# Optimization experiments

Measured on AMD Instinct MI355X. Metric: run time of the kernel, lower is better.

Reference implementation:

```python
import jax, jax.numpy as jnp
import numpy as np

FS = 30.0        # sampling rate (Hz)
HIGH_PASS = 40.0 # BPM
LOW_PASS = 250.0 # BPM


def setup_inputs() -> dict:
    key = jax.random.key(0)
    k1, k2 = jax.random.split(key)
    B, N = 1024, 16384
    outputs = jax.random.normal(k1, (B, N), dtype=jnp.float32)
    # heart rates in BPM, within (high_pass, low_pass) band so slices are non-degenerate
    targets = 45.0 + 150.0 * jax.random.uniform(k2, (B, 1), dtype=jnp.float32)
    return {"outputs": outputs, "targets": targets}


def reference(outputs, targets):
    N = outputs.shape[-1]
    F = N // 2 + 1
    pulse_band = jnp.array([HIGH_PASS / 60.0, LOW_PASS / 60.0], dtype=jnp.float32)
    f = jnp.linspace(0.0, FS / 2.0, F, dtype=jnp.float32)  # [F]
    min_idx = jnp.argmin(jnp.abs(f - pulse_band[0]))
    max_idx = jnp.argmin(jnp.abs(f - pulse_band[1]))

    outputs = outputs.reshape(-1, N)
    if targets.shape[-1] != 1:
        targets = jnp.mean(targets, axis=-1, keepdims=True)
    t_hz = targets.reshape(-1) / 60.0  # [B] target frequency in Hz

    # rfft with norm='forward' divides by N, matching torch.fft.rfft(norm='forward')
    X = jnp.fft.rfft(outputs, axis=-1, norm='forward')  # [B, F] complex
    P1 = X.real ** 2 + X.imag ** 2                       # [B, F] power spectrum

    # per-sample index of the reference (ground-truth) frequency bin
    ref_idx = jnp.argmin(jnp.abs(f[None, :] - t_hz[:, None]), axis=-1)  # [B]

    # vectorized masked reduction replacing the per-sample python loop:
    # sum over [min_idx, ref_idx-1) U [ref_idx+2, max_idx)
    j = jnp.arange(F)
    ri = ref_idx[:, None]
    mask = ((j[None, :] >= min_idx) & (j[None, :] < ri - 1)) | \
           ((j[None, :] >= ri + 2) & (j[None, :] < max_idx))
    other_sum = jnp.sum(jnp.where(mask, P1, 0.0), axis=-1)              # [B]
    denom = (max_idx - min_idx - 3).astype(jnp.float32)
    other_avrg = other_sum / denom

    pulse_freq_amp = jnp.take_along_axis(P1, ref_idx[:, None], axis=-1)[:, 0]  # [B]
    snrs = 10.0 * jnp.log10(pulse_freq_amp / other_avrg)
    return -jnp.mean(snrs)
```

## Files before the change

### kernel.cpp

```cpp
#include <hip/hip_runtime.h>
#include <math.h>

#define THREADS 512
#define MHALF 8192
#define NREAL 16384
#define MIN_IDX 364
#define MAX_IDX 2276

__device__ __forceinline__ int br13(int x) {
    return (int)(__brev((unsigned)x) >> 19);
}

__device__ __forceinline__ int PHI(int p) {
    return p ^ (((p >> 7) & 7) << 1);
}

__device__ __forceinline__ float2 wtw(float f) {
    return make_float2(__builtin_amdgcn_cosf(f), -__builtin_amdgcn_sinf(f));
}

__device__ __forceinline__ float2 cmul(float2 a, float2 b) {
    return make_float2(a.x * b.x - a.y * b.y, a.x * b.y + a.y * b.x);
}

__device__ __forceinline__ void bfly(float2& a, float2& b, float2 tw) {
    float2 t = make_float2(a.x - b.x, a.y - b.y);
    a.x += b.x; a.y += b.y;
    b = cmul(t, tw);
}

__device__ __forceinline__ void fft_block16(float2 v[16], float2 W1)
{
    constexpr float C16x[8] = {1.f,  0.92387953251128674f,  0.70710678118654757f,  0.38268343236508978f,
                               0.f, -0.38268343236508978f, -0.70710678118654757f, -0.92387953251128674f};
    constexpr float C16y[8] = {0.f, -0.38268343236508978f, -0.70710678118654757f, -0.92387953251128674f,
                              -1.f, -0.92387953251128674f, -0.70710678118654757f, -0.38268343236508978f};
    constexpr float C8x[4] = {1.f,  0.70710678118654757f,  0.f, -0.70710678118654757f};
    constexpr float C8y[4] = {0.f, -0.70710678118654757f, -1.f, -0.70710678118654757f};

    float2 W2 = cmul(W1, W1), W4 = cmul(W2, W2), W8 = cmul(W4, W4);

    #pragma unroll
    for (int m = 0; m < 8; ++m) {
        float2 tw = cmul(W1, make_float2(C16x[m], C16y[m]));
        bfly(v[m], v[m + 8], tw);
    }
    #pragma unroll
    for (int g = 0; g < 2; ++g) {
        #pragma unroll
        for (int m = 0; m < 4; ++m) {
            float2 tw = cmul(W2, make_float2(C8x[m], C8y[m]));
            bfly(v[8 * g + m], v[8 * g + m + 4], tw);
        }
    }
    float2 W4i = make_float2(W4.y, -W4.x);
    #pragma unroll
    for (int g = 0; g < 4; ++g) {
        bfly(v[4 * g + 0], v[4 * g + 2], W4);
        bfly(v[4 * g + 1], v[4 * g + 3], W4i);
    }
    #pragma unroll
    for (int g = 0; g < 8; ++g)
        bfly(v[2 * g], v[2 * g + 1], W8);
}

__global__ __launch_bounds__(THREADS, 2)
void negsnr_row_kernel(const float* __restrict__ x,
                       const float* __restrict__ targets,
                       float* __restrict__ snr_out)
{
    __shared__ float2 cf[MHALF];
    const int row  = blockIdx.x;
    const int tid  = threadIdx.x;
    const int lane = tid & 63;
    const int wave = tid >> 6;

    const float2* xr = (const float2*)(x + (size_t)row * NREAL);
    float2 v[16];
    #pragma unroll
    for (int m = 0; m < 16; ++m) v[m] = xr[tid + 512 * m];

    const float step = 15.0f / 8192.0f;
    const float t_hz = targets[row] / 60.0f;
    int ri;
    {
        int kf = (int)floorf(t_hz * (8192.0f / 15.0f));
        float best = 1e30f; ri = 0;
        #pragma unroll
        for (int d = -1; d <= 2; ++d) {
            int k = min(max(kf + d, 0), 8192);
            float dist = fabsf((float)k * step - t_hz);
            if (dist < best) { best = dist; ri = k; }
        }
    }

    fft_block16(v, wtw((float)tid * (1.0f / 8192.0f)));
    #pragma unroll
    for (int m = 0; m < 16; ++m) cf[PHI(tid + 512 * m)] = v[m];
    __syncthreads();

    const int low5 = tid & 31;
    const int base2 = low5 + ((tid >> 5) << 9);
    #pragma unroll
    for (int m = 0; m < 16; ++m) v[m] = cf[PHI(base2 + 32 * m)];
    fft_block16(v, wtw((float)low5 * (1.0f / 512.0f)));
    #pragma unroll
    for (int m = 0; m < 16; ++m) cf[PHI(base2 + 32 * m)] = v[m];
    __syncthreads();

    const int p = tid & 1;
    const int base3 = p + ((tid >> 1) << 5);
    #pragma unroll
    for (int m = 0; m < 16; ++m) v[m] = cf[PHI(base3 + 2 * m)];
    {
        float2 U = p ? make_float2(0.98078528040323044f, -0.19509032201612825f)
                     : make_float2(1.0f, 0.0f);
        fft_block16(v, U);
    }
    #pragma unroll
    for (int m = 0; m < 16; ++m) cf[PHI(base3 + 2 * m)] = v[m];
    __syncthreads();

    float other = 0.0f, pulse = 0.0f;
    bool hasp = false;
    for (int k = MIN_IDX + tid; k < MAX_IDX; k += THREADS) {
        int a = br13(k);
        int b = br13(MHALF - k);
        float4 ya = *(const float4*)&cf[PHI(a)];
        float4 yb = *(const float4*)&cf[PHI(b - 1)];
        float Zr  = ya.x + ya.z, Zi  = ya.y + ya.w;
        float Zmr = yb.x - yb.z, Zmi = yb.y - yb.w;
        float xer  = 0.5f * (Zr + Zmr), xei = 0.5f * (Zi - Zmi);
        float xor_ = 0.5f * (Zi + Zmi), xoi = -0.5f * (Zr - Zmr);
        float2 tw = wtw((float)k * (1.0f / 16384.0f));
        float xr_ = xer + tw.x * xor_ - tw.y * xoi;
        float xi_ = xei + tw.x * xoi + tw.y * xor_;
        float pw = xr_ * xr_ + xi_ * xi_;
        if (k < ri - 1 || k > ri + 1) other += pw;
        if (k == ri) { pulse = pw; hasp = true; }
    }
    __syncthreads();
    if (hasp) cf[8].x = pulse;
    #pragma unroll
    for (int off = 32; off; off >>= 1) other += __shfl_down(other, off);
    if (lane == 0) cf[wave].x = other;
    __syncthreads();
    if (tid == 0) {
        float tot = 0.0f;
        #pragma unroll
        for (int w = 0; w < 8; ++w) tot += cf[w].x;
        const float denom = (float)(MAX_IDX - MIN_IDX - 3);
        snr_out[row] = 10.0f * log10f(cf[8].x * denom / tot);
    }
}

__global__ void negsnr_mean_kernel(const float* __restrict__ snr,
                                   float* __restrict__ out, int n)
{
    __shared__ float sacc[4];
    const int tid = threadIdx.x;
    float acc = 0.0f;
    for (int i = tid; i < n; i += 256) acc += snr[i];
    #pragma unroll
    for (int off = 32; off; off >>= 1) acc += __shfl_down(acc, off);
    if ((tid & 63) == 0) sacc[tid >> 6] = acc;
    __syncthreads();
    if (tid == 0) {
        float t = sacc[0] + sacc[1] + sacc[2] + sacc[3];
        out[0] = -t / (float)n;
    }
}

extern "C" void kernel_launch(void* const* d_in, const int* in_sizes, int n_in,
                              void* d_out, int out_size, void* d_ws, size_t ws_size,
                              hipStream_t stream) {
    const float* outputs = (const float*)d_in[0];
    const float* targets = (const float*)d_in[1];
    const int B = in_sizes[1];
    float* snr = (float*)d_ws;

    negsnr_row_kernel<<<B, THREADS, 0, stream>>>(outputs, targets, snr);
    negsnr_mean_kernel<<<1, 256, 0, stream>>>(snr, (float*)d_out, B);
}
```

Measured before the change: 34.64 us.

## Store FFT intermediates in LDS as half2 to raise occupancy

Stores the shared-memory FFT exchange buffer as half2 instead of float2, halving LDS use per block. Launch bounds go from 2 to 8 blocks per CU, the LDS swizzle is changed to suit the new element size, and the final reduction moves to a separate small buffer so one barrier can be dropped. Rounding spectra to fp16 between stages loses precision and may cause overflow or underflow on large or small power values, which can shift the SNR result.

```diff
diff --git a/kernel.cpp b/kernel.cpp
--- a/kernel.cpp
+++ b/kernel.cpp
@@ -1,4 +1,5 @@
 #include <hip/hip_runtime.h>
+#include <hip/hip_fp16.h>
 #include <math.h>
 
 #define THREADS 512
@@ -12,7 +13,7 @@
 }
 
 __device__ __forceinline__ int PHI(int p) {
-    return p ^ (((p >> 7) & 7) << 1);
+    return p ^ ((p >> 5) & 31) ^ ((p >> 10) & 3);
 }
 
 __device__ __forceinline__ float2 wtw(float f) {
@@ -64,12 +65,13 @@
         bfly(v[2 * g], v[2 * g + 1], W8);
 }
 
-__global__ __launch_bounds__(THREADS, 2)
+__global__ __launch_bounds__(THREADS, 8)
 void negsnr_row_kernel(const float* __restrict__ x,
                        const float* __restrict__ targets,
                        float* __restrict__ snr_out)
 {
-    __shared__ float2 cf[MHALF];
+    __shared__ __half2 cf[MHALF];
+    __shared__ float   red[12];
     const int row  = blockIdx.x;
     const int tid  = threadIdx.x;
     const int lane = tid & 63;
@@ -96,29 +98,32 @@
 
     fft_block16(v, wtw((float)tid * (1.0f / 8192.0f)));
     #pragma unroll
-    for (int m = 0; m < 16; ++m) cf[PHI(tid + 512 * m)] = v[m];
+    for (int m = 0; m < 16; ++m)
+        cf[PHI(tid + 512 * m)] = __floats2half2_rn(v[m].x, v[m].y);
     __syncthreads();
 
     const int low5 = tid & 31;
     const int base2 = low5 + ((tid >> 5) << 9);
     #pragma unroll
-    for (int m = 0; m < 16; ++m) v[m] = cf[PHI(base2 + 32 * m)];
+    for (int m = 0; m < 16; ++m) v[m] = __half22float2(cf[PHI(base2 + 32 * m)]);
     fft_block16(v, wtw((float)low5 * (1.0f / 512.0f)));
     #pragma unroll
-    for (int m = 0; m < 16; ++m) cf[PHI(base2 + 32 * m)] = v[m];
+    for (int m = 0; m < 16; ++m)
+        cf[PHI(base2 + 32 * m)] = __floats2half2_rn(v[m].x, v[m].y);
     __syncthreads();
 
     const int p = tid & 1;
     const int base3 = p + ((tid >> 1) << 5);
     #pragma unroll
-    for (int m = 0; m < 16; ++m) v[m] = cf[PHI(base3 + 2 * m)];
+    for (int m = 0; m < 16; ++m) v[m] = __half22float2(cf[PHI(base3 + 2 * m)]);
     {
         float2 U = p ? make_float2(0.98078528040323044f, -0.19509032201612825f)
                      : make_float2(1.0f, 0.0f);
         fft_block16(v, U);
     }
     #pragma unroll
-    for (int m = 0; m < 16; ++m) cf[PHI(base3 + 2 * m)] = v[m];
+    for (int m = 0; m < 16; ++m)
+        cf[PHI(base3 + 2 * m)] = __floats2half2_rn(v[m].x, v[m].y);
     __syncthreads();
 
     float other = 0.0f, pulse = 0.0f;
@@ -126,10 +131,21 @@
     for (int k = MIN_IDX + tid; k < MAX_IDX; k += THREADS) {
         int a = br13(k);
         int b = br13(MHALF - k);
-        float4 ya = *(const float4*)&cf[PHI(a)];
-        float4 yb = *(const float4*)&cf[PHI(b - 1)];
-        float Zr  = ya.x + ya.z, Zi  = ya.y + ya.w;
-        float Zmr = yb.x - yb.z, Zmi = yb.y - yb.w;
+        int sa = PHI(a);
+        int sb = PHI(b - 1);
+        float2 e0 = __half22float2(cf[sa & ~1]);
+        float2 e1 = __half22float2(cf[sa | 1]);
+        bool swA = (sa & 1);
+        float2 Ya  = swA ? e1 : e0;
+        float2 Ya1 = swA ? e0 : e1;
+        float2 f0 = __half22float2(cf[sb & ~1]);
+        float2 f1 = __half22float2(cf[sb | 1]);
+        bool swB = (sb & 1);
+        float2 Yb1 = swB ? f1 : f0;
+        float2 Yb  = swB ? f0 : f1;
+
+        float Zr  = Ya.x + Ya1.x, Zi  = Ya.y + Ya1.y;
+        float Zmr = Yb1.x - Yb.x, Zmi = Yb1.y - Yb.y;
         float xer  = 0.5f * (Zr + Zmr), xei = 0.5f * (Zi - Zmi);
         float xor_ = 0.5f * (Zi + Zmi), xoi = -0.5f * (Zr - Zmr);
         float2 tw = wtw((float)k * (1.0f / 16384.0f));
@@ -139,18 +155,17 @@
         if (k < ri - 1 || k > ri + 1) other += pw;
         if (k == ri) { pulse = pw; hasp = true; }
     }
-    __syncthreads();
-    if (hasp) cf[8].x = pulse;
+    if (hasp) red[8] = pulse;
     #pragma unroll
     for (int off = 32; off; off >>= 1) other += __shfl_down(other, off);
-    if (lane == 0) cf[wave].x = other;
+    if (lane == 0) red[wave] = other;
     __syncthreads();
     if (tid == 0) {
         float tot = 0.0f;
         #pragma unroll
-        for (int w = 0; w < 8; ++w) tot += cf[w].x;
+        for (int w = 0; w < 8; ++w) tot += red[w];
         const float denom = (float)(MAX_IDX - MIN_IDX - 3);
-        snr_out[row] = 10.0f * log10f(cf[8].x * denom / tot);
+        snr_out[row] = 10.0f * log10f(red[8] * denom / tot);
     }
 }
 
```

Measured after the change: 107.5 us. 210% more time.
